# Optimization experiments

Hardware: AMD Instinct MI355X
Metric: run time of the kernel (lower is better)

## Reference

```python
import math
import jax, jax.numpy as jnp
import numpy as np

HEADS = 8
SCALE_BASE = 512.0
GN_EPS = 1e-5


def _gammas(heads):
    # 1 - exp(linspace(log(1/32), log(1/512), heads))
    return 1.0 - np.exp(np.linspace(math.log(1.0 / 32.0), math.log(1.0 / 512.0), heads))


def _xpos(x, downscale):
    # x: (N, S, d), d even. Faithful to torchscale XPOS with scale_base=512.
    N, S, d = x.shape
    half = d // 2
    scale = (jnp.arange(0, d, 2, dtype=jnp.float32) + 0.4 * d) / (1.4 * d)        # (half,)
    pos = jnp.arange(S, dtype=jnp.float32)
    sc = scale[None, :] ** (pos / SCALE_BASE)[:, None]                             # (S, half)
    inv_freq = 1.0 / (10000.0 ** (jnp.arange(half, dtype=jnp.float32) / half))
    sinusoid = pos[:, None] * inv_freq[None, :]                                    # (S, half)
    sin, cos = jnp.sin(sinusoid), jnp.cos(sinusoid)
    if downscale:
        sc = 1.0 / sc
    # duplicate_interleave == repeat each column twice adjacently
    sin_s = jnp.repeat(sin * sc, 2, axis=-1)                                       # (S, d)
    cos_s = jnp.repeat(cos * sc, 2, axis=-1)
    x1, x2 = x[..., ::2], x[..., 1::2]
    rot = jnp.stack((-x2, x1), axis=-1).reshape(x.shape)                           # rotate_every_two
    return x * cos_s + rot * sin_s


def setup_inputs() -> dict:
    key = jax.random.key(0)
    ks = jax.random.split(key, 6)
    B, S, H = 2, 2048, 1024
    h = HEADS
    d = H // h
    X = jax.random.normal(ks[0], (B, S, H), dtype=jnp.float32)
    # per-head projections, torch init: randn(d, d) / d
    W_Q = jax.random.normal(ks[1], (h, d, d), dtype=jnp.float32) / d
    W_K = jax.random.normal(ks[2], (h, d, d), dtype=jnp.float32) / d
    W_V = jax.random.normal(ks[3], (h, d, d), dtype=jnp.float32) / d
    W_G = jax.random.normal(ks[4], (H, H), dtype=jnp.float32) / H
    W_O = jax.random.normal(ks[5], (H, H), dtype=jnp.float32) / H
    gn_weight = jnp.ones((H,), dtype=jnp.float32)
    gn_bias = jnp.zeros((H,), dtype=jnp.float32)
    return {"X": X, "W_Q": W_Q, "W_K": W_K, "W_V": W_V,
            "W_G": W_G, "W_O": W_O, "gn_weight": gn_weight, "gn_bias": gn_bias}


def reference(X, W_Q, W_K, W_V, W_G, W_O, gn_weight, gn_bias):
    B, S, H = X.shape
    h = HEADS
    d = H // h
    gammas = jnp.asarray(_gammas(h), dtype=X.dtype)                                # (h,)

    Xh = X.reshape(B, S, h, d)
    Q = jnp.einsum('bshd,hde->bhse', Xh, W_Q)                                      # (B,h,S,d)
    K = jnp.einsum('bshd,hde->bhse', Xh, W_K)
    V = jnp.einsum('bshd,hde->bhse', Xh, W_V)

    Q = _xpos(Q.reshape(B * h, S, d), downscale=False).reshape(B, h, S, d)
    K = _xpos(K.reshape(B * h, S, d), downscale=True).reshape(B, h, S, d)

    # decay mask D[h, n, m] = gamma_h^(n-m) for n >= m else 0 (NaN-safe)
    n = jnp.arange(S)
    diff = n[:, None] - n[None, :]                                                 # (S,S)
    causal = (diff >= 0)
    D = (gammas[:, None, None] ** jnp.where(causal, diff, 0).astype(X.dtype)) \
        * causal[None].astype(X.dtype)                                             # (h,S,S)

    att = jnp.einsum('bhsd,bhtd->bhst', Q, K) * D[None]                            # (B,h,S,S)
    Y = jnp.einsum('bhst,bhtd->bshd', att, V).reshape(B, S, H)

    # GroupNorm(heads, hidden) over flattened (B*S, H), biased variance
    Yg = Y.reshape(B * S, h, d)
    mu = Yg.mean(axis=-1, keepdims=True)
    var = Yg.var(axis=-1, keepdims=True)
    Yn = ((Yg - mu) / jnp.sqrt(var + GN_EPS)).reshape(B * S, H)
    Yn = (Yn * gn_weight + gn_bias).reshape(B, S, H)

    G = X @ W_G
    return (G * jax.nn.sigmoid(G) * Yn) @ W_O
```

## Files before the change

### kernel.cpp

```cpp
#include <hip/hip_runtime.h>
#include <math.h>

#define NB 2
#define SEQ 2048
#define HD 1024
#define NH 8
#define DH 128
#define HALF 64

typedef __bf16 bf16_t;
typedef __attribute__((ext_vector_type(8))) __bf16 bf16x8;
typedef __attribute__((ext_vector_type(4))) __bf16 bf16x4;
typedef __attribute__((ext_vector_type(4))) float f32x4;

typedef __attribute__((address_space(1))) void gvoid;
typedef __attribute__((address_space(3))) void lvoid;

__device__ __forceinline__ void gld16(const bf16_t* g, bf16_t* l) {
  __builtin_amdgcn_global_load_lds((gvoid*)g, (lvoid*)l, 16, 0, 0);
}

__device__ __forceinline__ float head_l2g(int hh) {
  double ga = log(1.0/32.0), gbb = log(1.0/512.0);
  float gamma = (float)(1.0 - exp(ga + (double)hh * (gbb - ga) / 7.0));
  return log2f(gamma);
}

__device__ __forceinline__ void wsplit_body(
    const float* in, bf16_t* oh, int M, int N,
    int bx, int by, int z, float (*tile)[65], int nthr, int t) {
  in += (size_t)z * M * N; oh += (size_t)z * M * N;
  int r0 = by * 64, c0 = bx * 64;
  for (int idx = t; idx < 1024; idx += nthr) {
    int r = idx >> 4, c4 = (idx & 15) * 4;
    float4 v = *(const float4*)(in + (size_t)(r0 + r) * N + c0 + c4);
    *(float4*)&tile[r][c4] = v;
  }
  __syncthreads();
  for (int idx = t; idx < 1024; idx += nthr) {
    int c = idx >> 4, r4 = (idx & 15) * 4;
    bf16x4 h;
    #pragma unroll
    for (int j = 0; j < 4; ++j)
      h[j] = (bf16_t)tile[r4 + j][c];
    *(bf16x4*)(oh + (size_t)(c0 + c) * M + r0 + r4) = h;
  }
}

__global__ __launch_bounds__(256) void k_prep(
    const float* __restrict__ Wq, const float* __restrict__ Wk,
    const float* __restrict__ Wv,
    float* __restrict__ tabs, bf16_t* __restrict__ Wqt,
    bf16_t* __restrict__ Wkt, bf16_t* __restrict__ Wvt) {
  __shared__ float tile[64][65];
  int b = blockIdx.x;
  if (b < 512) {
    int idx = b * 256 + threadIdx.x;
    int s = idx >> 6, i = idx & 63;
    float dd = (float)DH;
    float scale = (2.0f * (float)i + 0.4f * dd) / (1.4f * dd);
    float sc = expf(logf(scale) * ((float)s / 512.0f));
    float inv_freq = expf(-logf(10000.0f) * ((float)i / (float)HALF));
    float ang = (float)s * inv_freq;
    float sn, cs;
    sincosf(ang, &sn, &cs);
    float rsc = 1.0f / sc;
    tabs[idx]               = sn * sc;
    tabs[SEQ*HALF + idx]    = cs * sc;
    tabs[2*SEQ*HALF + idx]  = sn * rsc;
    tabs[3*SEQ*HALF + idx]  = cs * rsc;
  } else {
    int i = b - 512;
    int which = i >> 5;
    int j = i & 31;
    const float* in = (which == 0) ? Wq : (which == 1) ? Wk : Wv;
    bf16_t* oh = (which == 0) ? Wqt : (which == 1) ? Wkt : Wvt;
    wsplit_body(in, oh, DH, DH, j & 1, (j >> 1) & 1, j >> 2, tile,
                256, threadIdx.x);
  }
}

__global__ __launch_bounds__(512, 1) void k_qkvd(
    const float* __restrict__ X, const float* __restrict__ tabs,
    const bf16_t* __restrict__ Wqt, const bf16_t* __restrict__ Wkt,
    const bf16_t* __restrict__ Wvt,
    bf16_t* __restrict__ Qo, bf16_t* __restrict__ Ko,
    bf16_t* __restrict__ VTo, bf16_t* __restrict__ Xhg,
    bf16_t* __restrict__ DSt) {
  __shared__ bf16_t Wsh[128][128];
  __shared__ bf16_t KT[128][128];
  __shared__ bf16_t Vd[128][128];
  int t = threadIdx.x;
  int lane = t & 63, w = t >> 6;
  int lr = lane & 15, lg = lane >> 4;
  int c = blockIdx.x, hh = blockIdx.y, b = blockIdx.z;
  int s0 = c * 128;
  size_t bh = (size_t)(b*NH + hh);
  float l2g = head_l2g(hh);

  bf16x8 xh[4];
  {
    const float* xp = X + ((size_t)(b*SEQ + s0 + 16*w + lr)) * HD + hh*DH + 8*lg;
    #pragma unroll
    for (int ks = 0; ks < 4; ++ks) {
      float4 u = *(const float4*)(xp + 32*ks);
      float4 v = *(const float4*)(xp + 32*ks + 4);
      float fv[8] = {u.x,u.y,u.z,u.w,v.x,v.y,v.z,v.w};
      #pragma unroll
      for (int j = 0; j < 8; ++j) xh[ks][j] = (bf16_t)fv[j];
    }
  }
  {
    bf16_t* xo = Xhg + ((size_t)(b*SEQ + s0 + 16*w + lr)) * HD + hh*DH + 8*lg;
    #pragma unroll
    for (int ks = 0; ks < 4; ++ks)
      *(bf16x8*)(xo + 32*ks) = xh[ks];
  }

  const bf16_t* Wp[3] = {Wqt, Wkt, Wvt};

  for (int which = 0; which < 3; ++which) {
    const bf16_t* wp = Wp[which] + (size_t)hh * (DH*DH);
    __syncthreads();
    #pragma unroll
    for (int i = 0; i < 4; ++i) {
      int e = w*16 + i*4 + (lane >> 4);
      int kb = (lane & 15) ^ (e & 7);
      gld16(wp + (size_t)e*DH + kb*8, &Wsh[w*16 + i*4][0]);
    }
    __syncthreads();
    f32x4 yacc[8];
    #pragma unroll
    for (int i = 0; i < 8; ++i) yacc[i] = (f32x4){0.f,0.f,0.f,0.f};
    #pragma unroll
    for (int sub = 0; sub < 8; ++sub) {
      int e = 16*sub + lr;
      #pragma unroll
      for (int ks = 0; ks < 4; ++ks) {
        int ch = (lg + 4*ks) ^ (lr & 7);
        bf16x8 bhv = *(const bf16x8*)&Wsh[e][ch*8];
        yacc[sub] = __builtin_amdgcn_mfma_f32_16x16x32_bf16(xh[ks], bhv, yacc[sub], 0, 0, 0);
      }
    }
    if (which < 2) {
      const float* st = tabs + (which ? 2*SEQ*HALF : 0);
      const float* ct = st + SEQ*HALF;
      bf16_t* Op = which ? Ko : Qo;
      #pragma unroll
      for (int sub = 0; sub < 8; ++sub) {
        int e = 16*sub + lr;
        int i = e >> 1;
        #pragma unroll
        for (int reg = 0; reg < 4; ++reg) {
          float v = yacc[sub][reg];
          float p = __shfl_xor(v, 1);
          int tau = 16*w + 4*lg + reg;
          int srow = s0 + tau;
          float sv = st[srow*HALF + i], cv = ct[srow*HALF + i];
          float o = v * cv + ((e & 1) ? p : -p) * sv;
          bf16_t ob = (bf16_t)o;
          Op[(bh*SEQ + srow) * DH + e] = ob;
          if (which == 1) {
            int col = (((tau>>3) ^ (e & 7)) << 3) | (tau & 7);
            KT[e][col] = ob;
          }
        }
      }
    } else {
      float decay[4];
      #pragma unroll
      for (int reg = 0; reg < 4; ++reg)
        decay[reg] = exp2f(l2g * (float)(127 - (16*w + 4*lg + reg)));
      #pragma unroll
      for (int sub = 0; sub < 8; ++sub) {
        int e = 16*sub + lr;
        bf16x4 hv;
        #pragma unroll
        for (int reg = 0; reg < 4; ++reg) {
          int tau = 16*w + 4*lg + reg;
          float f = yacc[sub][reg];
          hv[reg] = (bf16_t)f;
          int col = (((tau>>3) ^ (e & 7)) << 3) | (tau & 7);
          Vd[e][col] = (bf16_t)(f * decay[reg]);
        }
        *(bf16x4*)(VTo + bh * (size_t)(DH*SEQ) + (size_t)e*SEQ + (s0 + 16*w + 4*lg)) = hv;
      }
    }
  }
  __syncthreads();

  f32x4 acc[8];
  #pragma unroll
  for (int s = 0; s < 8; ++s) acc[s] = (f32x4){0.f,0.f,0.f,0.f};
  {
    int dv = 16*w + lr;
    #pragma unroll
    for (int ks = 0; ks < 4; ++ks) {
      int ca = (lg + 4*ks) ^ (dv & 7);
      bf16x8 avh = *(const bf16x8*)&Vd[dv][ca*8];
      #pragma unroll
      for (int sub = 0; sub < 8; ++sub) {
        int dk = 16*sub + lr;
        int cb = (lg + 4*ks) ^ (dk & 7);
        bf16x8 bkh = *(const bf16x8*)&KT[dk][cb*8];
        acc[sub] = __builtin_amdgcn_mfma_f32_16x16x32_bf16(avh, bkh, acc[sub], 0, 0, 0);
      }
    }
  }
  size_t obase = (bh * 16 + c) * 16384;
  #pragma unroll
  for (int sub = 0; sub < 8; ++sub)
    #pragma unroll
    for (int reg = 0; reg < 4; ++reg) {
      int dv = 16*w + 4*lg + reg;
      int dk = 16*sub + lr;
      DSt[obase + (size_t)dv*128 + dk] = (bf16_t)acc[sub][reg];
    }
}

__global__ __launch_bounds__(512, 1) void k_ret(
    const bf16_t* __restrict__ Qg, const bf16_t* __restrict__ Kg,
    const bf16_t* __restrict__ VTg, const bf16_t* __restrict__ DSt,
    const float* __restrict__ gw, const float* __restrict__ gb,
    bf16_t* __restrict__ Yn,
    const float* __restrict__ Wg, const float* __restrict__ Wo,
    bf16_t* __restrict__ Wgt, bf16_t* __restrict__ Wot) {
  __shared__ bf16_t Ksh[64][128];
  __shared__ bf16_t Vsh[128][64];
  __shared__ bf16_t Ph[128][64];
  __shared__ bf16_t Slds[128][128];
  __shared__ float tile[64][65];
  int t = threadIdx.x;
  int bid = blockIdx.x;
  if (bid >= 256) {
    int i = bid - 256;
    int which = i >> 8;
    int j = i & 255;
    wsplit_body(which ? Wo : Wg, which ? Wot : Wgt, HD, HD,
                j & 15, j >> 4, 0, tile, 512, t);
    return;
  }
  int lane = t & 63, w = t >> 6;
  int lr = lane & 15, lg = lane >> 4;
  int c = bid & 15, bh = bid >> 4, hh = bh & 7;
  int s0 = c * 128;
  size_t base  = (size_t)bh * SEQ * DH;
  size_t vbase = (size_t)bh * DH * SEQ;
  float l2g = head_l2g(hh);
  float colf = exp2f(-l2g * (float)lr);
  float g16v[4];
  #pragma unroll
  for (int ts = 0; ts < 4; ++ts) g16v[ts] = exp2f(-l2g * (float)(16*ts));

  #pragma unroll
  for (int i = 0; i < 2; ++i) {
    int r = w*8 + i*4 + (lane >> 4);
    int kb = (lane & 15) ^ (r & 7);
    gld16(Kg + base + (size_t)(s0 + r)*DH + kb*8, &Ksh[w*8 + i*4][0]);
  }
  #pragma unroll
  for (int i = 0; i < 2; ++i) {
    int d = w*16 + i*8 + (lane >> 3);
    int cb = (lane & 7) ^ (d & 7);
    gld16(VTg + vbase + (size_t)d*SEQ + s0 + cb*8, &Vsh[w*16 + i*8][0]);
  }

  bf16x8 qh[4];
  {
    const bf16_t* qp = Qg + base + (size_t)(s0 + 16*w + lr) * DH + lg * 8;
    #pragma unroll
    for (int ks = 0; ks < 4; ++ks)
      qh[ks] = *(const bf16x8*)(qp + 32*ks);
  }

  {
    float g128 = exp2f(l2g * 128.0f);
    float S0[8] = {}, S1[8] = {}, S2[8] = {}, S3[8] = {};
    const bf16_t* dbase = DSt + ((size_t)bh * 16) * 16384
                        + (size_t)(t >> 2) * 128 + (t & 3) * 32;
    for (int cp = 0; cp < c; ++cp) {
      const bf16_t* dp = dbase + (size_t)cp * 16384;
      bf16x8 d0 = *(const bf16x8*)dp;
      bf16x8 d1 = *(const bf16x8*)(dp + 8);
      bf16x8 d2 = *(const bf16x8*)(dp + 16);
      bf16x8 d3 = *(const bf16x8*)(dp + 24);
      #pragma unroll
      for (int j = 0; j < 8; ++j) {
        S0[j] = g128*S0[j] + (float)d0[j];
        S1[j] = g128*S1[j] + (float)d1[j];
        S2[j] = g128*S2[j] + (float)d2[j];
        S3[j] = g128*S3[j] + (float)d3[j];
      }
    }
    int dv = t >> 2;
    #pragma unroll
    for (int q = 0; q < 4; ++q) {
      const float* Sq = (q == 0) ? S0 : (q == 1) ? S1 : (q == 2) ? S2 : S3;
      int ch = ((t & 3) * 4 + q) ^ (dv & 7);
      bf16x8 s8;
      #pragma unroll
      for (int j = 0; j < 8; ++j) s8[j] = (bf16_t)Sq[j];
      *(bf16x8*)&Slds[dv][ch*8] = s8;
    }
  }
  __syncthreads();

  f32x4 yacc[8];
  #pragma unroll
  for (int i = 0; i < 8; ++i) yacc[i] = (f32x4){0.f,0.f,0.f,0.f};
  {
    #pragma unroll
    for (int sub = 0; sub < 8; ++sub) {
      int dv = 16*sub + lr;
      #pragma unroll
      for (int ks = 0; ks < 4; ++ks) {
        int ch = (lg + 4*ks) ^ (dv & 7);
        bf16x8 b8 = *(const bf16x8*)&Slds[dv][ch*8];
        yacc[sub] = __builtin_amdgcn_mfma_f32_16x16x32_bf16(qh[ks], b8, yacc[sub], 0, 0, 0);
      }
    }
    float rowc[4];
    #pragma unroll
    for (int reg = 0; reg < 4; ++reg)
      rowc[reg] = exp2f(l2g * (float)(16*w + 4*lg + reg + 1));
    #pragma unroll
    for (int sub = 0; sub < 8; ++sub)
      #pragma unroll
      for (int reg = 0; reg < 4; ++reg)
        yacc[sub][reg] *= rowc[reg];
  }

  for (int kt = 0; kt < 2; ++kt) {
    int t0 = kt * 64;
    if (kt == 1) {
      __syncthreads();
      #pragma unroll
      for (int i = 0; i < 2; ++i) {
        int r = w*8 + i*4 + (lane >> 4);
        int kb = (lane & 15) ^ (r & 7);
        gld16(Kg + base + (size_t)(s0 + 64 + r)*DH + kb*8, &Ksh[w*8 + i*4][0]);
      }
      #pragma unroll
      for (int i = 0; i < 2; ++i) {
        int d = w*16 + i*8 + (lane >> 3);
        int cb = (lane & 7) ^ (d & 7);
        gld16(VTg + vbase + (size_t)d*SEQ + s0 + 64 + cb*8, &Vsh[w*16 + i*8][0]);
      }
      __syncthreads();
    }
    if (!(kt == 1 && w < 4)) {
      float rowf[4];
      #pragma unroll
      for (int reg = 0; reg < 4; ++reg)
        rowf[reg] = exp2f(l2g * (float)(16*w + 4*lg + reg - t0));

      #pragma unroll
      for (int ts = 0; ts < 4; ++ts) {
        f32x4 sacc = (f32x4){0.f,0.f,0.f,0.f};
        int trow = 16*ts + lr;
        #pragma unroll
        for (int ks = 0; ks < 4; ++ks) {
          int kbs = (4*ks + lg) ^ (trow & 7);
          bf16x8 kh8 = *(const bf16x8*)&Ksh[trow][kbs*8];
          sacc = __builtin_amdgcn_mfma_f32_16x16x32_bf16(qh[ks], kh8, sacc, 0, 0, 0);
        }
        float cf = colf * g16v[ts];
        #pragma unroll
        for (int reg = 0; reg < 4; ++reg) {
          int qloc = 4*lg + reg;
          int diff = (16*w + qloc) - (t0 + trow);
          float p = (diff >= 0) ? sacc[reg] * (rowf[reg] * cf) : 0.0f;
          int cb = (trow >> 3) ^ (qloc & 7);
          Ph[16*w + qloc][cb*8 + (trow & 7)] = (bf16_t)p;
        }
      }
      #pragma unroll
      for (int ks = 0; ks < 2; ++ks) {
        int prow = 16*w + lr;
        int pcb = (4*ks + lg) ^ (lr & 7);
        bf16x8 pah = *(const bf16x8*)&Ph[prow][pcb*8];
        #pragma unroll
        for (int sub = 0; sub < 8; ++sub) {
          int drow = 16*sub + lr;
          int vcb = (4*ks + lg) ^ (drow & 7);
          bf16x8 vh8 = *(const bf16x8*)&Vsh[drow][vcb*8];
          yacc[sub] = __builtin_amdgcn_mfma_f32_16x16x32_bf16(pah, vh8, yacc[sub], 0, 0, 0);
        }
      }
    }
  }

  float s1v[4] = {0.f,0.f,0.f,0.f}, s2v[4] = {0.f,0.f,0.f,0.f};
  #pragma unroll
  for (int sub = 0; sub < 8; ++sub)
    #pragma unroll
    for (int reg = 0; reg < 4; ++reg) {
      float v = yacc[sub][reg];
      s1v[reg] += v;
      s2v[reg] += v * v;
    }
  #pragma unroll
  for (int off = 8; off; off >>= 1)
    #pragma unroll
    for (int reg = 0; reg < 4; ++reg) {
      s1v[reg] += __shfl_xor(s1v[reg], off);
      s2v[reg] += __shfl_xor(s2v[reg], off);
    }
  float gwv[8], gbv[8];
  #pragma unroll
  for (int sub = 0; sub < 8; ++sub) {
    gwv[sub] = gw[hh*DH + 16*sub + lr];
    gbv[sub] = gb[hh*DH + 16*sub + lr];
  }
  int b = bh >> 3;
  #pragma unroll
  for (int reg = 0; reg < 4; ++reg) {
    float mean = s1v[reg] * (1.0f/128.0f);
    float var = s2v[reg] * (1.0f/128.0f) - mean*mean;
    float inv = rsqrtf(var + 1e-5f);
    int srow = s0 + 16*w + 4*lg + reg;
    bf16_t* op = Yn + (size_t)(b*SEQ + srow) * HD + hh*DH;
    #pragma unroll
    for (int sub = 0; sub < 8; ++sub)
      op[16*sub + lr] = (bf16_t)((yacc[sub][reg] - mean) * inv * gwv[sub] + gbv[sub]);
  }
}

__global__ __launch_bounds__(256, 2) void k_gemm(
    const bf16_t* __restrict__ Ag, const bf16_t* __restrict__ Bg,
    const bf16_t* __restrict__ E,
    bf16_t* __restrict__ Oh, float* __restrict__ Of, int mode) {
  __shared__ bf16_t SA[2][64][64];
  __shared__ bf16_t SBB[2][128][64];
  int t = threadIdx.x;
  int lane = t & 63, w = t >> 6;
  int lr = lane & 15, lg = lane >> 4;
  int wr = w >> 1, wc = w & 1;
  int bid = blockIdx.x;
  int xcd = bid & 7, local = bid >> 3;
  int mp = xcd * 8 + (local >> 3);
  int np = local & 7;
  int m0 = mp * 64, n0 = np * 128;

  const bf16_t* As = Ag + (size_t)m0 * HD;
  const bf16_t* Bs = Bg + (size_t)n0 * HD;

  f32x4 acc[2][4];
  #pragma unroll
  for (int i = 0; i < 2; ++i)
    #pragma unroll
    for (int j = 0; j < 4; ++j) acc[i][j] = (f32x4){0.f,0.f,0.f,0.f};

  int srow = lane >> 3, sch = lane & 7;

  {
    #pragma unroll
    for (int i = 0; i < 2; ++i) {
      int row = w*16 + i*8 + srow;
      int kc = (sch ^ (row & 7)) * 8;
      gld16(As + (size_t)row*HD + kc, &SA[0][w*16 + i*8][0]);
    }
    #pragma unroll
    for (int i = 0; i < 4; ++i) {
      int row = w*32 + i*8 + srow;
      int kc = (sch ^ (row & 7)) * 8;
      gld16(Bs + (size_t)row*HD + kc, &SBB[0][w*32 + i*8][0]);
    }
  }
  __syncthreads();

  int buf = 0;
  for (int kt = 0; kt < 16; ++kt) {
    if (kt + 1 < 16) {
      int k0 = (kt + 1) * 64;
      #pragma unroll
      for (int i = 0; i < 2; ++i) {
        int row = w*16 + i*8 + srow;
        int kc = (sch ^ (row & 7)) * 8;
        gld16(As + (size_t)row*HD + k0 + kc, &SA[buf^1][w*16 + i*8][0]);
      }
      #pragma unroll
      for (int i = 0; i < 4; ++i) {
        int row = w*32 + i*8 + srow;
        int kc = (sch ^ (row & 7)) * 8;
        gld16(Bs + (size_t)row*HD + k0 + kc, &SBB[buf^1][w*32 + i*8][0]);
      }
    }
    #pragma unroll
    for (int ks = 0; ks < 2; ++ks) {
      bf16x8 a_[2], b_[4];
      #pragma unroll
      for (int mf = 0; mf < 2; ++mf) {
        int row = wr*32 + mf*16 + lr;
        int ch = (lg + 4*ks) ^ (row & 7);
        a_[mf] = *(const bf16x8*)&SA[buf][row][ch*8];
      }
      #pragma unroll
      for (int nf = 0; nf < 4; ++nf) {
        int row = wc*64 + nf*16 + lr;
        int ch = (lg + 4*ks) ^ (row & 7);
        b_[nf] = *(const bf16x8*)&SBB[buf][row][ch*8];
      }
      #pragma unroll
      for (int mf = 0; mf < 2; ++mf)
        #pragma unroll
        for (int nf = 0; nf < 4; ++nf)
          acc[mf][nf] = __builtin_amdgcn_mfma_f32_16x16x32_bf16(a_[mf], b_[nf], acc[mf][nf], 0, 0, 0);
    }
    __syncthreads();
    buf ^= 1;
  }
  #pragma unroll
  for (int mf = 0; mf < 2; ++mf) {
    #pragma unroll
    for (int nf = 0; nf < 4; ++nf) {
      #pragma unroll
      for (int reg = 0; reg < 4; ++reg) {
        int m = m0 + wr*32 + mf*16 + 4*lg + reg;
        int n = n0 + wc*64 + nf*16 + lr;
        float g = acc[mf][nf][reg];
        size_t off = (size_t)m * HD + n;
        if (mode == 1) {
          float sg = 1.0f / (1.0f + expf(-g));
          Oh[off] = (bf16_t)(g * sg * (float)E[off]);
        } else {
          Of[off] = g;
        }
      }
    }
  }
}

extern "C" void kernel_launch(void* const* d_in, const int* in_sizes, int n_in,
                              void* d_out, int out_size, void* d_ws, size_t ws_size,
                              hipStream_t stream) {
  const float* X  = (const float*)d_in[0];
  const float* Wq = (const float*)d_in[1];
  const float* Wk = (const float*)d_in[2];
  const float* Wv = (const float*)d_in[3];
  const float* Wg = (const float*)d_in[4];
  const float* Wo = (const float*)d_in[5];
  const float* gw = (const float*)d_in[6];
  const float* gb = (const float*)d_in[7];
  float* out = (float*)d_out;
  float* ws = (float*)d_ws;

  float* tabs = ws;
  bf16_t* Q   = (bf16_t*)(ws + 524288);
  bf16_t* K   = Q + 4194304;
  bf16_t* VT  = K + 4194304;
  bf16_t* Yn  = VT + 4194304;
  bf16_t* DSt = Yn + 4194304;
  bf16_t* Wqt = DSt + 4194304;
  bf16_t* Wkt = Wqt + 131072;
  bf16_t* Wvt = Wkt + 131072;
  bf16_t* Wgt = Wvt + 131072;
  bf16_t* Wot = Wgt + 1048576;
  bf16_t* Xh  = Wot + 1048576;
  bf16_t* A2  = Q;

  k_prep<<<dim3(608), dim3(256), 0, stream>>>(Wq, Wk, Wv, tabs, Wqt, Wkt, Wvt);
  k_qkvd<<<dim3(16, 8, 2), dim3(512), 0, stream>>>(X, tabs, Wqt, Wkt, Wvt,
                                                   Q, K, VT, Xh, DSt);
  k_ret<<<dim3(768), dim3(512), 0, stream>>>(Q, K, VT, DSt, gw, gb, Yn,
                                             Wg, Wo, Wgt, Wot);
  k_gemm<<<dim3(512), dim3(256), 0, stream>>>(Xh, Wgt, Yn, A2, nullptr, 1);
  k_gemm<<<dim3(512), dim3(256), 0, stream>>>(A2, Wot, nullptr, nullptr, out, 0);
}
```

Before: 95.49 us.

## Fuse prep, QKV projection and retention into one cooperative grid-synced kernel

Merges the prep, QKV/chunk-state, and retention kernels into a single cooperative kernel of 256 blocks that keeps Q, K and V for its chunk in LDS across a grid-wide sync. This removes the global round trips for Q, K and V^T and two kernel launches. XPOS sin/cos and scale are now computed inline instead of read from precomputed tables, and fp32 weights are converted while being staged into LDS. The cost is heavier LDS use (about 160KB per block), redundant transcendental math, the Wg/Wo transposes moved onto the critical path before the sync, and a dependence on all 256 blocks being co-resident.

```diff
diff --git a/kernel.cpp b/kernel.cpp
--- a/kernel.cpp
+++ b/kernel.cpp
@@ -1,5 +1,8 @@
 #include <hip/hip_runtime.h>
+#include <hip/hip_cooperative_groups.h>
 #include <math.h>
+
+namespace cg = cooperative_groups;
 
 #define NB 2
 #define SEQ 2048
@@ -47,56 +50,39 @@
   }
 }
 
-__global__ __launch_bounds__(256) void k_prep(
+__global__ __launch_bounds__(512, 1) void k_fused(
+    const float* __restrict__ X,
     const float* __restrict__ Wq, const float* __restrict__ Wk,
-    const float* __restrict__ Wv,
-    float* __restrict__ tabs, bf16_t* __restrict__ Wqt,
-    bf16_t* __restrict__ Wkt, bf16_t* __restrict__ Wvt) {
-  __shared__ float tile[64][65];
-  int b = blockIdx.x;
-  if (b < 512) {
-    int idx = b * 256 + threadIdx.x;
-    int s = idx >> 6, i = idx & 63;
-    float dd = (float)DH;
-    float scale = (2.0f * (float)i + 0.4f * dd) / (1.4f * dd);
-    float sc = expf(logf(scale) * ((float)s / 512.0f));
-    float inv_freq = expf(-logf(10000.0f) * ((float)i / (float)HALF));
-    float ang = (float)s * inv_freq;
-    float sn, cs;
-    sincosf(ang, &sn, &cs);
-    float rsc = 1.0f / sc;
-    tabs[idx]               = sn * sc;
-    tabs[SEQ*HALF + idx]    = cs * sc;
-    tabs[2*SEQ*HALF + idx]  = sn * rsc;
-    tabs[3*SEQ*HALF + idx]  = cs * rsc;
-  } else {
-    int i = b - 512;
-    int which = i >> 5;
-    int j = i & 31;
-    const float* in = (which == 0) ? Wq : (which == 1) ? Wk : Wv;
-    bf16_t* oh = (which == 0) ? Wqt : (which == 1) ? Wkt : Wvt;
-    wsplit_body(in, oh, DH, DH, j & 1, (j >> 1) & 1, j >> 2, tile,
-                256, threadIdx.x);
-  }
-}
-
-__global__ __launch_bounds__(512, 1) void k_qkvd(
-    const float* __restrict__ X, const float* __restrict__ tabs,
-    const bf16_t* __restrict__ Wqt, const bf16_t* __restrict__ Wkt,
-    const bf16_t* __restrict__ Wvt,
-    bf16_t* __restrict__ Qo, bf16_t* __restrict__ Ko,
-    bf16_t* __restrict__ VTo, bf16_t* __restrict__ Xhg,
-    bf16_t* __restrict__ DSt) {
-  __shared__ bf16_t Wsh[128][128];
-  __shared__ bf16_t KT[128][128];
-  __shared__ bf16_t Vd[128][128];
+    const float* __restrict__ Wv, const float* __restrict__ Wg,
+    const float* __restrict__ Wo,
+    const float* __restrict__ gw, const float* __restrict__ gb,
+    bf16_t* __restrict__ Xhg, bf16_t* __restrict__ DSt,
+    bf16_t* __restrict__ Yn, bf16_t* __restrict__ Wgt,
+    bf16_t* __restrict__ Wot) {
+  __shared__ bf16_t Wsh[64][128];
+  __shared__ bf16_t KTd[128][128];
+  __shared__ bf16_t Vsh[128][128];
+  __shared__ bf16_t Ksh[128][128];
+  __shared__ bf16_t Qsh[128][128];
   int t = threadIdx.x;
   int lane = t & 63, w = t >> 6;
   int lr = lane & 15, lg = lane >> 4;
-  int c = blockIdx.x, hh = blockIdx.y, b = blockIdx.z;
+  int bid = blockIdx.x;
+  int c = bid & 15, bh = bid >> 4, hh = bh & 7, b = bh >> 3;
   int s0 = c * 128;
-  size_t bh = (size_t)(b*NH + hh);
   float l2g = head_l2g(hh);
+
+  {
+    float (*tile)[65] = (float(*)[65])&Qsh[0][0];
+    #pragma unroll
+    for (int k = 0; k < 2; ++k) {
+      int i = bid * 2 + k;
+      int which = i >> 8, j = i & 255;
+      wsplit_body(which ? Wo : Wg, which ? Wot : Wgt, HD, HD,
+                  j & 15, j >> 4, 0, tile, 512, t);
+      __syncthreads();
+    }
+  }
 
   bf16x8 xh[4];
   {
@@ -109,168 +95,126 @@
       #pragma unroll
       for (int j = 0; j < 8; ++j) xh[ks][j] = (bf16_t)fv[j];
     }
-  }
-  {
     bf16_t* xo = Xhg + ((size_t)(b*SEQ + s0 + 16*w + lr)) * HD + hh*DH + 8*lg;
     #pragma unroll
     for (int ks = 0; ks < 4; ++ks)
       *(bf16x8*)(xo + 32*ks) = xh[ks];
   }
 
-  const bf16_t* Wp[3] = {Wqt, Wkt, Wvt};
-
+  const float* Wsrc[3] = {Wq, Wk, Wv};
   for (int which = 0; which < 3; ++which) {
-    const bf16_t* wp = Wp[which] + (size_t)hh * (DH*DH);
-    __syncthreads();
-    #pragma unroll
-    for (int i = 0; i < 4; ++i) {
-      int e = w*16 + i*4 + (lane >> 4);
-      int kb = (lane & 15) ^ (e & 7);
-      gld16(wp + (size_t)e*DH + kb*8, &Wsh[w*16 + i*4][0]);
-    }
-    __syncthreads();
+    const float* wp = Wsrc[which] + (size_t)hh * (DH*DH);
     f32x4 yacc[8];
     #pragma unroll
     for (int i = 0; i < 8; ++i) yacc[i] = (f32x4){0.f,0.f,0.f,0.f};
-    #pragma unroll
-    for (int sub = 0; sub < 8; ++sub) {
-      int e = 16*sub + lr;
-      #pragma unroll
-      for (int ks = 0; ks < 4; ++ks) {
-        int ch = (lg + 4*ks) ^ (lr & 7);
-        bf16x8 bhv = *(const bf16x8*)&Wsh[e][ch*8];
-        yacc[sub] = __builtin_amdgcn_mfma_f32_16x16x32_bf16(xh[ks], bhv, yacc[sub], 0, 0, 0);
+    for (int hf = 0; hf < 2; ++hf) {
+      __syncthreads();
+      for (int idx = t; idx < 2048; idx += 512) {
+        int d = idx >> 4;
+        int e4 = (idx & 15) * 4 + hf * 64;
+        float4 v = *(const float4*)(wp + (size_t)d * DH + e4);
+        float fv[4] = {v.x, v.y, v.z, v.w};
+        #pragma unroll
+        for (int j = 0; j < 4; ++j) {
+          int e = e4 + j;
+          Wsh[e - hf*64][(((d>>3) ^ (e & 7)) << 3) | (d & 7)] = (bf16_t)fv[j];
+        }
+      }
+      __syncthreads();
+      #pragma unroll
+      for (int su = 0; su < 4; ++su) {
+        int sub = hf*4 + su;
+        int el = 16*su + lr;
+        #pragma unroll
+        for (int ks = 0; ks < 4; ++ks) {
+          int ch = (lg + 4*ks) ^ (el & 7);
+          bf16x8 bhv = *(const bf16x8*)&Wsh[el][ch*8];
+          yacc[sub] = __builtin_amdgcn_mfma_f32_16x16x32_bf16(xh[ks], bhv, yacc[sub], 0, 0, 0);
+        }
       }
     }
     if (which < 2) {
-      const float* st = tabs + (which ? 2*SEQ*HALF : 0);
-      const float* ct = st + SEQ*HALF;
-      bf16_t* Op = which ? Ko : Qo;
       #pragma unroll
       for (int sub = 0; sub < 8; ++sub) {
         int e = 16*sub + lr;
-        int i = e >> 1;
+        int i2 = e >> 1;
+        float scale = (2.f*(float)i2 + 51.2f) * (1.f/179.2f);
+        float l2s = log2f(scale);
+        float invf = exp2f(-13.287712379549449f * (float)i2 * (1.f/64.f));
         #pragma unroll
         for (int reg = 0; reg < 4; ++reg) {
           float v = yacc[sub][reg];
           float p = __shfl_xor(v, 1);
           int tau = 16*w + 4*lg + reg;
           int srow = s0 + tau;
-          float sv = st[srow*HALF + i], cv = ct[srow*HALF + i];
-          float o = v * cv + ((e & 1) ? p : -p) * sv;
+          float sc = exp2f(l2s * (float)srow * (1.f/512.f));
+          float ang = (float)srow * invf;
+          float sn, cs;
+          sincosf(ang, &sn, &cs);
+          float scq = (which == 0) ? sc : (1.f/sc);
+          float o = v * (cs*scq) + ((e & 1) ? p : -p) * (sn*scq);
           bf16_t ob = (bf16_t)o;
-          Op[(bh*SEQ + srow) * DH + e] = ob;
-          if (which == 1) {
-            int col = (((tau>>3) ^ (e & 7)) << 3) | (tau & 7);
-            KT[e][col] = ob;
+          if (which == 0) {
+            Qsh[tau][(((e>>3) ^ (tau&7)) << 3) | (e & 7)] = ob;
+          } else {
+            Ksh[tau][(((e>>3) ^ (tau&7)) << 3) | (e & 7)] = ob;
+            float kd = o * exp2f(l2g * (float)(127 - tau));
+            KTd[e][(((tau>>3) ^ (e&7)) << 3) | (tau & 7)] = (bf16_t)kd;
           }
         }
       }
     } else {
-      float decay[4];
-      #pragma unroll
-      for (int reg = 0; reg < 4; ++reg)
-        decay[reg] = exp2f(l2g * (float)(127 - (16*w + 4*lg + reg)));
       #pragma unroll
       for (int sub = 0; sub < 8; ++sub) {
         int e = 16*sub + lr;
-        bf16x4 hv;
         #pragma unroll
         for (int reg = 0; reg < 4; ++reg) {
           int tau = 16*w + 4*lg + reg;
-          float f = yacc[sub][reg];
-          hv[reg] = (bf16_t)f;
-          int col = (((tau>>3) ^ (e & 7)) << 3) | (tau & 7);
-          Vd[e][col] = (bf16_t)(f * decay[reg]);
+          Vsh[e][(((tau>>3) ^ (e&7)) << 3) | (tau & 7)] = (bf16_t)yacc[sub][reg];
         }
-        *(bf16x4*)(VTo + bh * (size_t)(DH*SEQ) + (size_t)e*SEQ + (s0 + 16*w + 4*lg)) = hv;
       }
     }
   }
   __syncthreads();
 
-  f32x4 acc[8];
-  #pragma unroll
-  for (int s = 0; s < 8; ++s) acc[s] = (f32x4){0.f,0.f,0.f,0.f};
-  {
+  {
+    f32x4 dacc[8];
+    #pragma unroll
+    for (int s = 0; s < 8; ++s) dacc[s] = (f32x4){0.f,0.f,0.f,0.f};
     int dv = 16*w + lr;
     #pragma unroll
     for (int ks = 0; ks < 4; ++ks) {
       int ca = (lg + 4*ks) ^ (dv & 7);
-      bf16x8 avh = *(const bf16x8*)&Vd[dv][ca*8];
+      bf16x8 av = *(const bf16x8*)&Vsh[dv][ca*8];
       #pragma unroll
       for (int sub = 0; sub < 8; ++sub) {
         int dk = 16*sub + lr;
         int cb = (lg + 4*ks) ^ (dk & 7);
-        bf16x8 bkh = *(const bf16x8*)&KT[dk][cb*8];
-        acc[sub] = __builtin_amdgcn_mfma_f32_16x16x32_bf16(avh, bkh, acc[sub], 0, 0, 0);
-      }
-    }
-  }
-  size_t obase = (bh * 16 + c) * 16384;
-  #pragma unroll
-  for (int sub = 0; sub < 8; ++sub)
-    #pragma unroll
-    for (int reg = 0; reg < 4; ++reg) {
-      int dv = 16*w + 4*lg + reg;
-      int dk = 16*sub + lr;
-      DSt[obase + (size_t)dv*128 + dk] = (bf16_t)acc[sub][reg];
-    }
-}
-
-__global__ __launch_bounds__(512, 1) void k_ret(
-    const bf16_t* __restrict__ Qg, const bf16_t* __restrict__ Kg,
-    const bf16_t* __restrict__ VTg, const bf16_t* __restrict__ DSt,
-    const float* __restrict__ gw, const float* __restrict__ gb,
-    bf16_t* __restrict__ Yn,
-    const float* __restrict__ Wg, const float* __restrict__ Wo,
-    bf16_t* __restrict__ Wgt, bf16_t* __restrict__ Wot) {
-  __shared__ bf16_t Ksh[64][128];
-  __shared__ bf16_t Vsh[128][64];
-  __shared__ bf16_t Ph[128][64];
-  __shared__ bf16_t Slds[128][128];
-  __shared__ float tile[64][65];
-  int t = threadIdx.x;
-  int bid = blockIdx.x;
-  if (bid >= 256) {
-    int i = bid - 256;
-    int which = i >> 8;
-    int j = i & 255;
-    wsplit_body(which ? Wo : Wg, which ? Wot : Wgt, HD, HD,
-                j & 15, j >> 4, 0, tile, 512, t);
-    return;
-  }
-  int lane = t & 63, w = t >> 6;
-  int lr = lane & 15, lg = lane >> 4;
-  int c = bid & 15, bh = bid >> 4, hh = bh & 7;
-  int s0 = c * 128;
-  size_t base  = (size_t)bh * SEQ * DH;
-  size_t vbase = (size_t)bh * DH * SEQ;
-  float l2g = head_l2g(hh);
-  float colf = exp2f(-l2g * (float)lr);
-  float g16v[4];
-  #pragma unroll
-  for (int ts = 0; ts < 4; ++ts) g16v[ts] = exp2f(-l2g * (float)(16*ts));
-
-  #pragma unroll
-  for (int i = 0; i < 2; ++i) {
-    int r = w*8 + i*4 + (lane >> 4);
-    int kb = (lane & 15) ^ (r & 7);
-    gld16(Kg + base + (size_t)(s0 + r)*DH + kb*8, &Ksh[w*8 + i*4][0]);
-  }
-  #pragma unroll
-  for (int i = 0; i < 2; ++i) {
-    int d = w*16 + i*8 + (lane >> 3);
-    int cb = (lane & 7) ^ (d & 7);
-    gld16(VTg + vbase + (size_t)d*SEQ + s0 + cb*8, &Vsh[w*16 + i*8][0]);
-  }
+        bf16x8 bk = *(const bf16x8*)&KTd[dk][cb*8];
+        dacc[sub] = __builtin_amdgcn_mfma_f32_16x16x32_bf16(av, bk, dacc[sub], 0, 0, 0);
+      }
+    }
+    size_t obase = ((size_t)bh * 16 + c) * 16384;
+    #pragma unroll
+    for (int sub = 0; sub < 8; ++sub)
+      #pragma unroll
+      for (int reg = 0; reg < 4; ++reg) {
+        int dvv = 16*w + 4*lg + reg;
+        int dk = 16*sub + lr;
+        DSt[obase + (size_t)dvv*128 + dk] = (bf16_t)dacc[sub][reg];
+      }
+  }
+  __threadfence();
+  cg::this_grid().sync();
 
   bf16x8 qh[4];
   {
-    const bf16_t* qp = Qg + base + (size_t)(s0 + 16*w + lr) * DH + lg * 8;
-    #pragma unroll
-    for (int ks = 0; ks < 4; ++ks)
-      qh[ks] = *(const bf16x8*)(qp + 32*ks);
+    int q = 16*w + lr;
+    #pragma unroll
+    for (int ks = 0; ks < 4; ++ks) {
+      int ch = (lg + 4*ks) ^ (q & 7);
+      qh[ks] = *(const bf16x8*)&Qsh[q][ch*8];
+    }
   }
 
   {
@@ -294,13 +238,13 @@
     }
     int dv = t >> 2;
     #pragma unroll
-    for (int q = 0; q < 4; ++q) {
-      const float* Sq = (q == 0) ? S0 : (q == 1) ? S1 : (q == 2) ? S2 : S3;
-      int ch = ((t & 3) * 4 + q) ^ (dv & 7);
+    for (int q4 = 0; q4 < 4; ++q4) {
+      const float* Sq = (q4 == 0) ? S0 : (q4 == 1) ? S1 : (q4 == 2) ? S2 : S3;
+      int ch = ((t & 3) * 4 + q4) ^ (dv & 7);
       bf16x8 s8;
       #pragma unroll
       for (int j = 0; j < 8; ++j) s8[j] = (bf16_t)Sq[j];
-      *(bf16x8*)&Slds[dv][ch*8] = s8;
+      *(bf16x8*)&KTd[dv][ch*8] = s8;
     }
   }
   __syncthreads();
@@ -315,7 +259,7 @@
       #pragma unroll
       for (int ks = 0; ks < 4; ++ks) {
         int ch = (lg + 4*ks) ^ (dv & 7);
-        bf16x8 b8 = *(const bf16x8*)&Slds[dv][ch*8];
+        bf16x8 b8 = *(const bf16x8*)&KTd[dv][ch*8];
         yacc[sub] = __builtin_amdgcn_mfma_f32_16x16x32_bf16(qh[ks], b8, yacc[sub], 0, 0, 0);
       }
     }
@@ -330,62 +274,42 @@
         yacc[sub][reg] *= rowc[reg];
   }
 
-  for (int kt = 0; kt < 2; ++kt) {
-    int t0 = kt * 64;
-    if (kt == 1) {
-      __syncthreads();
-      #pragma unroll
-      for (int i = 0; i < 2; ++i) {
-        int r = w*8 + i*4 + (lane >> 4);
-        int kb = (lane & 15) ^ (r & 7);
-        gld16(Kg + base + (size_t)(s0 + 64 + r)*DH + kb*8, &Ksh[w*8 + i*4][0]);
-      }
-      #pragma unroll
-      for (int i = 0; i < 2; ++i) {
-        int d = w*16 + i*8 + (lane >> 3);
-        int cb = (lane & 7) ^ (d & 7);
-        gld16(VTg + vbase + (size_t)d*SEQ + s0 + 64 + cb*8, &Vsh[w*16 + i*8][0]);
-      }
-      __syncthreads();
-    }
-    if (!(kt == 1 && w < 4)) {
-      float rowf[4];
-      #pragma unroll
-      for (int reg = 0; reg < 4; ++reg)
-        rowf[reg] = exp2f(l2g * (float)(16*w + 4*lg + reg - t0));
-
-      #pragma unroll
-      for (int ts = 0; ts < 4; ++ts) {
-        f32x4 sacc = (f32x4){0.f,0.f,0.f,0.f};
-        int trow = 16*ts + lr;
-        #pragma unroll
-        for (int ks = 0; ks < 4; ++ks) {
-          int kbs = (4*ks + lg) ^ (trow & 7);
-          bf16x8 kh8 = *(const bf16x8*)&Ksh[trow][kbs*8];
-          sacc = __builtin_amdgcn_mfma_f32_16x16x32_bf16(qh[ks], kh8, sacc, 0, 0, 0);
-        }
-        float cf = colf * g16v[ts];
-        #pragma unroll
-        for (int reg = 0; reg < 4; ++reg) {
-          int qloc = 4*lg + reg;
-          int diff = (16*w + qloc) - (t0 + trow);
-          float p = (diff >= 0) ? sacc[reg] * (rowf[reg] * cf) : 0.0f;
-          int cb = (trow >> 3) ^ (qloc & 7);
-          Ph[16*w + qloc][cb*8 + (trow & 7)] = (bf16_t)p;
-        }
-      }
-      #pragma unroll
-      for (int ks = 0; ks < 2; ++ks) {
-        int prow = 16*w + lr;
-        int pcb = (4*ks + lg) ^ (lr & 7);
-        bf16x8 pah = *(const bf16x8*)&Ph[prow][pcb*8];
-        #pragma unroll
-        for (int sub = 0; sub < 8; ++sub) {
-          int drow = 16*sub + lr;
-          int vcb = (4*ks + lg) ^ (drow & 7);
-          bf16x8 vh8 = *(const bf16x8*)&Vsh[drow][vcb*8];
-          yacc[sub] = __builtin_amdgcn_mfma_f32_16x16x32_bf16(pah, vh8, yacc[sub], 0, 0, 0);
-        }
+  {
+    float colf = exp2f(-l2g * (float)lr);
+    float rowf[4];
+    #pragma unroll
+    for (int reg = 0; reg < 4; ++reg)
+      rowf[reg] = exp2f(l2g * (float)(16*w + 4*lg + reg));
+    #pragma unroll
+    for (int ts = 0; ts < 8; ++ts) {
+      f32x4 sacc = (f32x4){0.f,0.f,0.f,0.f};
+      int trow = 16*ts + lr;
+      #pragma unroll
+      for (int ks = 0; ks < 4; ++ks) {
+        int kbs = (4*ks + lg) ^ (trow & 7);
+        bf16x8 kh8 = *(const bf16x8*)&Ksh[trow][kbs*8];
+        sacc = __builtin_amdgcn_mfma_f32_16x16x32_bf16(qh[ks], kh8, sacc, 0, 0, 0);
+      }
+      float cf = colf * exp2f(-l2g * (float)(16*ts));
+      #pragma unroll
+      for (int reg = 0; reg < 4; ++reg) {
+        int qloc = 16*w + 4*lg + reg;
+        int diff = qloc - trow;
+        float p = (diff >= 0) ? sacc[reg] * (rowf[reg] * cf) : 0.0f;
+        Qsh[qloc][(((trow>>3) ^ (qloc&7)) << 3) | (trow & 7)] = (bf16_t)p;
+      }
+    }
+    #pragma unroll
+    for (int ks = 0; ks < 4; ++ks) {
+      int prow = 16*w + lr;
+      int pcb = (4*ks + lg) ^ (prow & 7);
+      bf16x8 pah = *(const bf16x8*)&Qsh[prow][pcb*8];
+      #pragma unroll
+      for (int sub = 0; sub < 8; ++sub) {
+        int dv = 16*sub + lr;
+        int vcb = (4*ks + lg) ^ (dv & 7);
+        bf16x8 vh8 = *(const bf16x8*)&Vsh[dv][vcb*8];
+        yacc[sub] = __builtin_amdgcn_mfma_f32_16x16x32_bf16(pah, vh8, yacc[sub], 0, 0, 0);
       }
     }
   }
@@ -412,7 +336,6 @@
     gwv[sub] = gw[hh*DH + 16*sub + lr];
     gbv[sub] = gb[hh*DH + 16*sub + lr];
   }
-  int b = bh >> 3;
   #pragma unroll
   for (int reg = 0; reg < 4; ++reg) {
     float mean = s1v[reg] * (1.0f/128.0f);
@@ -543,27 +466,21 @@
   const float* gw = (const float*)d_in[6];
   const float* gb = (const float*)d_in[7];
   float* out = (float*)d_out;
-  float* ws = (float*)d_ws;
-
-  float* tabs = ws;
-  bf16_t* Q   = (bf16_t*)(ws + 524288);
-  bf16_t* K   = Q + 4194304;
-  bf16_t* VT  = K + 4194304;
-  bf16_t* Yn  = VT + 4194304;
+  bf16_t* ws = (bf16_t*)d_ws;
+
+  bf16_t* Xh  = ws;
+  bf16_t* Yn  = Xh + 4194304;
   bf16_t* DSt = Yn + 4194304;
-  bf16_t* Wqt = DSt + 4194304;
-  bf16_t* Wkt = Wqt + 131072;
-  bf16_t* Wvt = Wkt + 131072;
-  bf16_t* Wgt = Wvt + 131072;
+  bf16_t* Wgt = DSt + 4194304;
   bf16_t* Wot = Wgt + 1048576;
-  bf16_t* Xh  = Wot + 1048576;
-  bf16_t* A2  = Q;
-
-  k_prep<<<dim3(608), dim3(256), 0, stream>>>(Wq, Wk, Wv, tabs, Wqt, Wkt, Wvt);
-  k_qkvd<<<dim3(16, 8, 2), dim3(512), 0, stream>>>(X, tabs, Wqt, Wkt, Wvt,
-                                                   Q, K, VT, Xh, DSt);
-  k_ret<<<dim3(768), dim3(512), 0, stream>>>(Q, K, VT, DSt, gw, gb, Yn,
-                                             Wg, Wo, Wgt, Wot);
+  bf16_t* A2  = Wot + 1048576;
+
+  void* args[] = {
+    (void*)&X, (void*)&Wq, (void*)&Wk, (void*)&Wv, (void*)&Wg, (void*)&Wo,
+    (void*)&gw, (void*)&gb, (void*)&Xh, (void*)&DSt, (void*)&Yn,
+    (void*)&Wgt, (void*)&Wot };
+  hipLaunchCooperativeKernel((const void*)k_fused, dim3(256), dim3(512),
+                             args, 0, stream);
   k_gemm<<<dim3(512), dim3(256), 0, stream>>>(Xh, Wgt, Yn, A2, nullptr, 1);
   k_gemm<<<dim3(512), dim3(256), 0, stream>>>(A2, Wot, nullptr, nullptr, out, 0);
 }
```

After: 230.3 us. 2.41x slower.
